# Kernel optimization log

Measured on AMD Instinct MI355X. Metric: run time of the kernel, lower is better.

## Reference

```python
import jax, jax.numpy as jnp
import numpy as np

B, T, D = 4, 2048, 1024
H, K, V = 4, 256, 256        # head_k_dim = head_v_dim = hidden/num_heads
M, TOPK = 256, 4             # num_slots == head_k_dim
CHUNK = 64                   # scan checkpointing granularity
SCALE = K ** -0.5            # kernel default q scale


def setup_inputs() -> dict:
    key = jax.random.key(0)
    ks = jax.random.split(key, 10)
    s = lambda i, shape, sc: jax.random.normal(ks[i], shape, jnp.float32) * sc
    return {
        "hidden_states": s(0, (B, T, D), 1.0),
        "Wq": s(1, (D, H * K), D ** -0.5),
        "Wk": s(2, (D, H * K), D ** -0.5),
        "Wv": s(3, (D, H * V), D ** -0.5),
        "Wa": s(4, (D, H), D ** -0.5),
        "Wr": s(5, (D, H * M), D ** -0.5),
        "Wb": s(6, (D, H), D ** -0.5),
        "dt": jax.random.uniform(ks[7], (H,), jnp.float32, np.log(0.001), np.log(0.1)),
        "norm_w": jnp.ones((V,), jnp.float32),
        "Wo": s(8, (H * V, D), (H * V) ** -0.5),
    }


def _l2norm(x):
    return x * jax.lax.rsqrt(jnp.sum(x * x, axis=-1, keepdims=True) + 1e-6)


def _delta_scan(q, k, v, g, beta):
    """Gated delta-rule recurrence. Time-major inputs:
    q,k,g: [T,B,H,K]; v: [T,B,H,V]; beta: [T,B,H]. Returns o: [T,B,H,V]."""
    def step(S, inp):
        qt, kt, vt, gt, bt = inp
        S = S * jnp.exp(gt)[..., None]                              # diag decay on key dim
        err = vt - jnp.einsum('bhk,bhkv->bhv', kt, S)               # delta-rule error
        S = S + kt[..., None] * (bt[..., None] * err)[..., None, :]
        o = jnp.einsum('bhk,bhkv->bhv', qt, S)
        return S, o

    @jax.checkpoint
    def chunk_fn(S, inp):
        return jax.lax.scan(step, S, inp)

    nc = T // CHUNK
    inp = tuple(x.reshape((nc, CHUNK) + x.shape[1:]) for x in (q, k, v, g, beta))
    S0 = jnp.zeros((B, H, K, V), jnp.float32)
    _, o = jax.lax.scan(chunk_fn, S0, inp)                          # o: [nc,CHUNK,B,H,V]
    return o.reshape((T,) + o.shape[2:])


def reference(hidden_states, Wq, Wk, Wv, Wa, Wr, Wb, dt, norm_w, Wo):
    h = hidden_states
    q = jax.nn.silu(h @ Wq).reshape(B, T, H, K)
    k = jax.nn.silu(h @ Wk).reshape(B, T, H, K)
    v = jax.nn.silu(h @ Wv).reshape(B, T, H, V)
    a = -jax.nn.softplus(h @ Wa) * jnp.exp(dt)                      # [B,T,H] log-decay magnitude
    rt = (h @ Wr).reshape(B, T, H, M)
    beta = jax.nn.sigmoid(h @ Wb)                                   # [B,T,H]

    # noisy top-k slot routing (eval: no noise)
    m = jax.nn.sigmoid(rt)
    w, idx = jax.lax.top_k(m, TOPK)                                 # [B,T,H,TOPK]
    mask = jnp.sum(jax.nn.one_hot(idx, M, dtype=m.dtype) * w[..., None], axis=-2)
    r = mask / (jnp.sum(mask, axis=-1, keepdims=True) + 1e-6)
    g = a[..., None] * r                                            # [B,T,H,K] (M == K)

    k = k * (1.0 - jnp.exp(g))
    q = _l2norm(q) * SCALE
    k = _l2norm(k)

    tm = lambda x: jnp.moveaxis(x, 1, 0)
    o = _delta_scan(tm(q), tm(k), tm(v), tm(g), tm(beta))           # [T,B,H,V]
    o = jnp.moveaxis(o, 0, 1)                                       # [B,T,H,V]

    # RMSNorm on head_v_dim (fp32, eps 1e-5)
    o = o * jax.lax.rsqrt(jnp.mean(o * o, axis=-1, keepdims=True) + 1e-5) * norm_w
    return o.reshape(B, T, H * V) @ Wo
```

## Files before the change

### kernel.cpp

```cpp
#include <hip/hip_runtime.h>
#include <hip/hip_bf16.h>

#define TT 2048
#define BB 4
#define HH 4
#define DD 1024

using bf16x8 = __attribute__((ext_vector_type(8))) short;
using f32x4  = __attribute__((ext_vector_type(4))) float;

__device__ __forceinline__ float wave_sum(float x) {
#pragma unroll
  for (int off = 32; off >= 1; off >>= 1) x += __shfl_xor(x, off);
  return x;
}

__device__ __forceinline__ float siluf(float x) {
  return x / (1.f + expf(-x));
}

__device__ __forceinline__ unsigned short f2bf(float f) {
  unsigned u = __float_as_uint(f);
  u = (u + 0x7fffu + ((u >> 16) & 1u)) >> 16;
  return (unsigned short)u;
}
__device__ __forceinline__ float bf2f(unsigned short b) {
  return __uint_as_float(((unsigned)b) << 16);
}
__device__ __forceinline__ unsigned pack2(float a, float b) {
  return ((unsigned)f2bf(a)) | (((unsigned)f2bf(b)) << 16);
}

__device__ __forceinline__ void gload_lds16(const void* g, void* l) {
  __builtin_amdgcn_global_load_lds(
      (const __attribute__((address_space(1))) unsigned int*)g,
      (__attribute__((address_space(3))) unsigned int*)l, 16, 0, 0);
}

#define LBAR()                                              \
  do {                                                      \
    asm volatile("s_waitcnt lgkmcnt(0)" ::: "memory");      \
    __builtin_amdgcn_s_barrier();                           \
    __builtin_amdgcn_sched_barrier(0);                      \
  } while (0)

__global__ __launch_bounds__(256) void gemm_bt(const unsigned short* __restrict__ A,
                                               const unsigned short* __restrict__ Bt,
                                               float* __restrict__ C,
                                               int M, int N, int K) {
  __shared__ unsigned short As[128 * 64];
  __shared__ unsigned short Bs[128 * 64];
  const int tid = threadIdx.x;
  const int l = tid & 63;
  const int w = tid >> 6;
  const int wm = w >> 1, wn = w & 1;
  const int bid = blockIdx.x;
  const int nt = N >> 7;
  const int swz = (bid & 7) * ((int)gridDim.x >> 3) + (bid >> 3);
  const int m0 = (swz / nt) * 128, n0 = (swz % nt) * 128;

  f32x4 acc[4][4];
#pragma unroll
  for (int i = 0; i < 4; ++i)
#pragma unroll
    for (int j = 0; j < 4; ++j) acc[i][j] = (f32x4){0.f, 0.f, 0.f, 0.f};

  size_t asrc[4], bsrc[4];
  int ldst[4];
#pragma unroll
  for (int it = 0; it < 4; ++it) {
    int chunk = (it * 4 + w) * 64 + l;
    int row = chunk >> 3, s = chunk & 7;
    size_t soff = (size_t)row * K + ((s ^ (row & 7)) << 3);
    asrc[it] = (size_t)m0 * K + soff;
    bsrc[it] = (size_t)n0 * K + soff;
    ldst[it] = chunk * 8;
  }
  int ra_off[2][4], rb_off[2][4];
#pragma unroll
  for (int kh = 0; kh < 2; ++kh)
#pragma unroll
    for (int f = 0; f < 4; ++f) {
      int rowA = wm * 64 + f * 16 + (l & 15);
      ra_off[kh][f] = rowA * 128 + (((kh * 4 + (l >> 4)) ^ (rowA & 7)) << 4);
      int rowB = wn * 64 + f * 16 + (l & 15);
      rb_off[kh][f] = rowB * 128 + (((kh * 4 + (l >> 4)) ^ (rowB & 7)) << 4);
    }

  for (int k0 = 0; k0 < K; k0 += 64) {
    __syncthreads();
#pragma unroll
    for (int it = 0; it < 4; ++it) {
      gload_lds16(A + asrc[it] + k0, As + ldst[it] - l * 8);
      gload_lds16(Bt + bsrc[it] + k0, Bs + ldst[it] - l * 8);
    }
    __syncthreads();
#pragma unroll
    for (int kh = 0; kh < 2; ++kh) {
      bf16x8 af[4], bfv[4];
#pragma unroll
      for (int f = 0; f < 4; ++f) {
        af[f] = *(const bf16x8*)((const char*)As + ra_off[kh][f]);
        bfv[f] = *(const bf16x8*)((const char*)Bs + rb_off[kh][f]);
      }
#pragma unroll
      for (int i = 0; i < 4; ++i)
#pragma unroll
        for (int j = 0; j < 4; ++j)
          acc[i][j] = __builtin_amdgcn_mfma_f32_16x16x32_bf16(af[i], bfv[j],
                                                              acc[i][j], 0, 0, 0);
    }
  }
  const int cn = n0 + wn * 64 + (l & 15);
  const int rbase = m0 + wm * 64 + ((l >> 4) << 2);
#pragma unroll
  for (int i = 0; i < 4; ++i)
#pragma unroll
    for (int j = 0; j < 4; ++j)
#pragma unroll
      for (int r = 0; r < 4; ++r)
        C[(size_t)(rbase + i * 16 + r) * N + cn + j * 16] = acc[i][j][r];
}

__global__ __launch_bounds__(256) void gemm_bt3(const unsigned short* __restrict__ Ah,
                                                const unsigned short* __restrict__ Al,
                                                const unsigned short* __restrict__ Bh,
                                                const unsigned short* __restrict__ Bl,
                                                float* __restrict__ C,
                                                int M, int N, int K) {
  __shared__ unsigned short Ash[128 * 64];
  __shared__ unsigned short Asl[128 * 64];
  __shared__ unsigned short Bsh[128 * 64];
  __shared__ unsigned short Bsl[128 * 64];
  const int tid = threadIdx.x;
  const int l = tid & 63;
  const int w = tid >> 6;
  const int wm = w >> 1, wn = w & 1;
  const int bid = blockIdx.x;
  const int nt = N >> 7;
  const int swz = (bid & 7) * ((int)gridDim.x >> 3) + (bid >> 3);
  const int m0 = (swz / nt) * 128, n0 = (swz % nt) * 128;

  f32x4 acc[4][4];
#pragma unroll
  for (int i = 0; i < 4; ++i)
#pragma unroll
    for (int j = 0; j < 4; ++j) acc[i][j] = (f32x4){0.f, 0.f, 0.f, 0.f};

  size_t asrc[4], bsrc[4];
  int ldst[4];
#pragma unroll
  for (int it = 0; it < 4; ++it) {
    int chunk = (it * 4 + w) * 64 + l;
    int row = chunk >> 3, s = chunk & 7;
    size_t soff = (size_t)row * K + ((s ^ (row & 7)) << 3);
    asrc[it] = (size_t)m0 * K + soff;
    bsrc[it] = (size_t)n0 * K + soff;
    ldst[it] = chunk * 8;
  }
  int ra_off[2][4], rb_off[2][4];
#pragma unroll
  for (int kh = 0; kh < 2; ++kh)
#pragma unroll
    for (int f = 0; f < 4; ++f) {
      int rowA = wm * 64 + f * 16 + (l & 15);
      ra_off[kh][f] = rowA * 128 + (((kh * 4 + (l >> 4)) ^ (rowA & 7)) << 4);
      int rowB = wn * 64 + f * 16 + (l & 15);
      rb_off[kh][f] = rowB * 128 + (((kh * 4 + (l >> 4)) ^ (rowB & 7)) << 4);
    }

  for (int k0 = 0; k0 < K; k0 += 64) {
    __syncthreads();
#pragma unroll
    for (int it = 0; it < 4; ++it) {
      gload_lds16(Ah + asrc[it] + k0, Ash + ldst[it] - l * 8);
      gload_lds16(Al + asrc[it] + k0, Asl + ldst[it] - l * 8);
      gload_lds16(Bh + bsrc[it] + k0, Bsh + ldst[it] - l * 8);
      gload_lds16(Bl + bsrc[it] + k0, Bsl + ldst[it] - l * 8);
    }
    __syncthreads();
#pragma unroll
    for (int kh = 0; kh < 2; ++kh) {
      bf16x8 afh[4], bfh[4], tmp[4];
#pragma unroll
      for (int f = 0; f < 4; ++f) {
        afh[f] = *(const bf16x8*)((const char*)Ash + ra_off[kh][f]);
        bfh[f] = *(const bf16x8*)((const char*)Bsh + rb_off[kh][f]);
      }
#pragma unroll
      for (int i = 0; i < 4; ++i)
#pragma unroll
        for (int j = 0; j < 4; ++j)
          acc[i][j] = __builtin_amdgcn_mfma_f32_16x16x32_bf16(afh[i], bfh[j],
                                                              acc[i][j], 0, 0, 0);
#pragma unroll
      for (int f = 0; f < 4; ++f)
        tmp[f] = *(const bf16x8*)((const char*)Asl + ra_off[kh][f]);
#pragma unroll
      for (int i = 0; i < 4; ++i)
#pragma unroll
        for (int j = 0; j < 4; ++j)
          acc[i][j] = __builtin_amdgcn_mfma_f32_16x16x32_bf16(tmp[i], bfh[j],
                                                              acc[i][j], 0, 0, 0);
#pragma unroll
      for (int f = 0; f < 4; ++f)
        tmp[f] = *(const bf16x8*)((const char*)Bsl + rb_off[kh][f]);
#pragma unroll
      for (int i = 0; i < 4; ++i)
#pragma unroll
        for (int j = 0; j < 4; ++j)
          acc[i][j] = __builtin_amdgcn_mfma_f32_16x16x32_bf16(afh[i], tmp[j],
                                                              acc[i][j], 0, 0, 0);
    }
  }
  const int cn = n0 + wn * 64 + (l & 15);
  const int rbase = m0 + wm * 64 + ((l >> 4) << 2);
#pragma unroll
  for (int i = 0; i < 4; ++i)
#pragma unroll
    for (int j = 0; j < 4; ++j)
#pragma unroll
      for (int r = 0; r < 4; ++r)
        C[(size_t)(rbase + i * 16 + r) * N + cn + j * 16] = acc[i][j][r];
}

__global__ __launch_bounds__(256) void cast_bf16_kernel(const float* __restrict__ in,
                                                        unsigned short* __restrict__ out) {
  const size_t i = ((size_t)blockIdx.x * 256 + threadIdx.x) * 4;
  float4 x = *(const float4*)(in + i);
  ushort4 o4;
  o4.x = f2bf(x.x);
  o4.y = f2bf(x.y);
  o4.z = f2bf(x.z);
  o4.w = f2bf(x.w);
  *(ushort4*)(out + i) = o4;
}

__global__ __launch_bounds__(256) void cast2_bf16_kernel(const float* __restrict__ in,
                                                         unsigned short* __restrict__ hi,
                                                         unsigned short* __restrict__ lo) {
  const size_t i = ((size_t)blockIdx.x * 256 + threadIdx.x) * 4;
  float4 x = *(const float4*)(in + i);
  ushort4 h4, l4;
  h4.x = f2bf(x.x); l4.x = f2bf(x.x - bf2f(h4.x));
  h4.y = f2bf(x.y); l4.y = f2bf(x.y - bf2f(h4.y));
  h4.z = f2bf(x.z); l4.z = f2bf(x.z - bf2f(h4.z));
  h4.w = f2bf(x.w); l4.w = f2bf(x.w - bf2f(h4.w));
  *(ushort4*)(hi + i) = h4;
  *(ushort4*)(lo + i) = l4;
}

__global__ __launch_bounds__(256) void tcast_kernel(const float* __restrict__ W,
                                                    unsigned short* __restrict__ WT,
                                                    int R, int C) {
  __shared__ float tile[32][33];
  const int tx = threadIdx.x, ty = threadIdx.y;
  const int c0 = blockIdx.x * 32, r0 = blockIdx.y * 32;
#pragma unroll
  for (int i = 0; i < 4; ++i)
    tile[ty + 8 * i][tx] = W[(size_t)(r0 + ty + 8 * i) * C + c0 + tx];
  __syncthreads();
#pragma unroll
  for (int i = 0; i < 4; ++i)
    WT[(size_t)(c0 + ty + 8 * i) * R + r0 + tx] = f2bf(tile[tx][ty + 8 * i]);
}

__global__ __launch_bounds__(256) void tcast2_kernel(const float* __restrict__ W,
                                                     unsigned short* __restrict__ WTh,
                                                     unsigned short* __restrict__ WTl,
                                                     int R, int C) {
  __shared__ float tile[32][33];
  const int tx = threadIdx.x, ty = threadIdx.y;
  const int c0 = blockIdx.x * 32, r0 = blockIdx.y * 32;
#pragma unroll
  for (int i = 0; i < 4; ++i)
    tile[ty + 8 * i][tx] = W[(size_t)(r0 + ty + 8 * i) * C + c0 + tx];
  __syncthreads();
#pragma unroll
  for (int i = 0; i < 4; ++i) {
    float x = tile[tx][ty + 8 * i];
    unsigned short h = f2bf(x);
    WTh[(size_t)(c0 + ty + 8 * i) * R + r0 + tx] = h;
    WTl[(size_t)(c0 + ty + 8 * i) * R + r0 + tx] = f2bf(x - bf2f(h));
  }
}

__global__ __launch_bounds__(256) void routing_kernel(
    const float* __restrict__ hidden, const float* __restrict__ Wa,
    const float* __restrict__ Wb, const float* __restrict__ dt,
    const float* __restrict__ rproj, float* __restrict__ qk,
    float* __restrict__ kk_, float* __restrict__ vv, float* __restrict__ gbuf,
    float* __restrict__ betaT) {
  const int row = blockIdx.x;
  const int b = row >> 11;
  const int t = row & (TT - 1);
  const int h = threadIdx.x >> 6;
  const int l = threadIdx.x & 63;
  const size_t base = (size_t)row * DD + h * 256;

  const float* hrow = hidden + (size_t)row * DD;
  float aa = 0.f, bb = 0.f;
#pragma unroll
  for (int i = 0; i < 16; ++i) {
    float hv = hrow[l + 64 * i];
    aa = fmaf(hv, Wa[(l + 64 * i) * HH + h], aa);
    bb = fmaf(hv, Wb[(l + 64 * i) * HH + h], bb);
  }
  aa = wave_sum(aa);
  bb = wave_sum(bb);
  float sp = (aa > 20.f) ? aa : log1pf(expf(aa));
  float a_ = -sp * expf(dt[h]);
  float beta = 1.f / (1.f + expf(-bb));
  const int bh = b * HH + h;
  if (l == 0) betaT[(size_t)bh * TT + t] = beta;

  float4 rt4 = *(const float4*)(rproj + base + l * 4);
  float rv[4] = {rt4.x, rt4.y, rt4.z, rt4.w};
  int used = 0;
  int widx[4];
  float wsig[4], wg[4], wkfac[4];
#pragma unroll
  for (int it = 0; it < 4; ++it) {
    float bv = -3.4e38f;
    int bi = 0x7fffffff;
#pragma unroll
    for (int c = 0; c < 4; ++c) {
      bool ok = !(used & (1 << c));
      float v = rv[c];
      if (ok && (v > bv)) {
        bv = v;
        bi = l * 4 + c;
      }
    }
#pragma unroll
    for (int off = 32; off >= 1; off >>= 1) {
      float ov = __shfl_xor(bv, off);
      int oi = __shfl_xor(bi, off);
      if (ov > bv || (ov == bv && oi < bi)) {
        bv = ov;
        bi = oi;
      }
    }
    widx[it] = bi;
    wsig[it] = 1.f / (1.f + expf(-bv));
    if ((bi >> 2) == l) used |= 1 << (bi & 3);
  }
  float wsum = wsig[0] + wsig[1] + wsig[2] + wsig[3] + 1e-6f;
#pragma unroll
  for (int it = 0; it < 4; ++it) {
    float g = a_ * (wsig[it] / wsum);
    wg[it] = g;
    wkfac[it] = 1.f - expf(g);
  }

  float4 kv4 = *(const float4*)(kk_ + base + l * 4);
  float kvv[4] = {kv4.x, kv4.y, kv4.z, kv4.w};
  float kmask[4], ddv[4];
#pragma unroll
  for (int c = 0; c < 4; ++c) {
    int slot = l * 4 + c;
    float f = 0.f, d = 0.f;
#pragma unroll
    for (int it = 0; it < 4; ++it) {
      bool hit = (slot == widx[it]);
      f = hit ? wkfac[it] : f;
      d = hit ? wg[it] : d;
    }
    kmask[c] = siluf(kvv[c]) * f;
    ddv[c] = d;
  }
  float ss = kmask[0] * kmask[0] + kmask[1] * kmask[1] + kmask[2] * kmask[2] +
             kmask[3] * kmask[3];
  ss = wave_sum(ss);
  float kn = rsqrtf(ss + 1e-6f);
  *(float4*)(kk_ + base + l * 4) =
      make_float4(kmask[0] * kn, kmask[1] * kn, kmask[2] * kn, kmask[3] * kn);
  *(float4*)(gbuf + ((size_t)bh * TT + t) * 256 + l * 4) =
      make_float4(ddv[0], ddv[1], ddv[2], ddv[3]);

  float4 qv4 = *(const float4*)(qk + base + l * 4);
  float qs[4] = {siluf(qv4.x), siluf(qv4.y), siluf(qv4.z), siluf(qv4.w)};
  float qss = qs[0] * qs[0] + qs[1] * qs[1] + qs[2] * qs[2] + qs[3] * qs[3];
  qss = wave_sum(qss);
  float qn = rsqrtf(qss + 1e-6f) * 0.0625f;
  *(float4*)(qk + base + l * 4) =
      make_float4(qs[0] * qn, qs[1] * qn, qs[2] * qn, qs[3] * qn);

  float4 vv4 = *(const float4*)(vv + base + l * 4);
  *(float4*)(vv + base + l * 4) =
      make_float4(siluf(vv4.x), siluf(vv4.y), siluf(vv4.z), siluf(vv4.w));
}

__global__ __launch_bounds__(256) void phaseA_kernel(
    const float* __restrict__ kproj, const float* __restrict__ qproj,
    float* __restrict__ expcG,
    const float* __restrict__ betaT, unsigned short* __restrict__ TinvB,
    unsigned short* __restrict__ AB, unsigned short* __restrict__ Wg,
    unsigned short* __restrict__ Qg, unsigned short* __restrict__ XTg) {
  __shared__ unsigned short XB[64 * 256];
  __shared__ unsigned short QW[128 * 256];
  __shared__ float Mb[64 * 68];
  const int bid = blockIdx.x;
  const int bh = bid >> 5, c = bid & 31;
  const int b = bh >> 2, h = bh & 3;
  const int t0 = c * 64;
  const int tid = threadIdx.x;
  const int w = tid >> 6, l = tid & 63;
  const int ln = l & 15, lg = l >> 4;

  {
    float cacc = 0.f;
    const int slot = tid >> 3, byt = tid & 7;
#pragma unroll 4
    for (int i = 0; i < 64; ++i) {
      size_t ga = ((size_t)bh * TT + t0 + i) * 256 + tid;
      size_t pa = (((size_t)b * TT + t0 + i) * HH + h) * 256 + tid;
      cacc += expcG[ga];
      float e = expf(cacc);
      float ei = __builtin_amdgcn_rcpf(e);
      float kv = kproj[pa], qv = qproj[pa];
      unsigned short wb = f2bf(kv * e);
      unsigned short qb = f2bf(qv * e);
      unsigned short xb = f2bf(kv * ei);
      Wg[ga] = wb;
      Qg[ga] = qb;
      int sw = ((slot ^ (i & 7)) << 3) + byt;
      XB[i * 256 + sw] = xb;
      QW[i * 256 + sw] = qb;
      QW[(i + 64) * 256 + sw] = wb;
      if (i == 63) expcG[ga] = e;
    }
  }
  __syncthreads();

  f32x4 acc[2][4];
#pragma unroll
  for (int tr = 0; tr < 2; ++tr)
#pragma unroll
    for (int tc = 0; tc < 4; ++tc) acc[tr][tc] = (f32x4){0.f, 0.f, 0.f, 0.f};
  const int R0 = w * 32;
#pragma unroll
  for (int kt = 0; kt < 8; ++kt) {
    const int ks = kt * 4 + lg;
    const int ra0 = R0 + ln, ra1 = R0 + 16 + ln;
    bf16x8 a0 = *(const bf16x8*)&QW[ra0 * 256 + ((ks ^ (ra0 & 7)) << 3)];
    bf16x8 a1 = *(const bf16x8*)&QW[ra1 * 256 + ((ks ^ (ra1 & 7)) << 3)];
#pragma unroll
    for (int tc = 0; tc < 4; ++tc) {
      const int br = tc * 16 + ln;
      bf16x8 bf_ = *(const bf16x8*)&XB[br * 256 + ((ks ^ (br & 7)) << 3)];
      acc[0][tc] = __builtin_amdgcn_mfma_f32_16x16x32_bf16(a0, bf_, acc[0][tc], 0, 0, 0);
      acc[1][tc] = __builtin_amdgcn_mfma_f32_16x16x32_bf16(a1, bf_, acc[1][tc], 0, 0, 0);
    }
  }
  const size_t gb = (((size_t)bh * 32 + c) << 12);
  if (w < 2) {
#pragma unroll
    for (int tr = 0; tr < 2; ++tr)
#pragma unroll
      for (int tc = 0; tc < 4; ++tc)
#pragma unroll
        for (int r = 0; r < 4; ++r) {
          int i = R0 + tr * 16 + lg * 4 + r;
          int s = tc * 16 + ln;
          AB[gb + i * 64 + s] = (s <= i) ? f2bf(acc[tr][tc][r]) : (unsigned short)0;
        }
  } else {
#pragma unroll
    for (int tr = 0; tr < 2; ++tr)
#pragma unroll
      for (int tc = 0; tc < 4; ++tc)
#pragma unroll
        for (int r = 0; r < 4; ++r) {
          int i = R0 - 64 + tr * 16 + lg * 4 + r;
          Mb[i * 68 + tc * 16 + ln] = acc[tr][tc][r];
        }
  }
  __syncthreads();

  if (w == 0) {
    float tcol[64];
#pragma unroll
    for (int i = 0; i < 64; ++i) {
      float bi = betaT[(size_t)bh * TT + t0 + i];
      float a_ = (l == i) ? 1.f : 0.f;
#pragma unroll
      for (int s = 0; s < i; ++s)
        a_ = fmaf(-bi * Mb[i * 68 + s], tcol[s], a_);
      tcol[i] = a_;
    }
#pragma unroll
    for (int s = 0; s < 64; ++s) Mb[s * 68 + l] = tcol[s];
  } else {
    const int kk1 = tid - 64;
#pragma unroll 1
    for (int pass = 0; pass < 2; ++pass) {
      if (pass == 1 && kk1 >= 64) break;
      const int k = (pass == 0) ? kk1 : (192 + kk1);
      unsigned short* dst = XTg + ((size_t)bh * 256 + k) * TT + t0;
      const int kslot = k >> 3, kb = k & 7;
#pragma unroll 1
      for (int jq = 0; jq < 8; ++jq) {
        unsigned short e[8];
#pragma unroll
        for (int j = 0; j < 8; ++j) {
          int t = jq * 8 + j;
          e[j] = XB[t * 256 + (((kslot ^ (t & 7)) << 3) + kb)];
        }
        uint4 o;
        o.x = ((unsigned)e[0]) | (((unsigned)e[1]) << 16);
        o.y = ((unsigned)e[2]) | (((unsigned)e[3]) << 16);
        o.z = ((unsigned)e[4]) | (((unsigned)e[5]) << 16);
        o.w = ((unsigned)e[6]) | (((unsigned)e[7]) << 16);
        *(uint4*)(dst + jq * 8) = o;
      }
    }
  }
  __syncthreads();
  {
    const int i = tid >> 2;
    const int sb = (tid & 3) * 16;
#pragma unroll
    for (int mq = 0; mq < 4; ++mq) {
      float v0 = Mb[i * 68 + sb + mq * 4 + 0];
      float v1 = Mb[i * 68 + sb + mq * 4 + 1];
      float v2 = Mb[i * 68 + sb + mq * 4 + 2];
      float v3 = Mb[i * 68 + sb + mq * 4 + 3];
      uint2 p;
      p.x = pack2(v0, v1);
      p.y = pack2(v2, v3);
      *(uint2*)(TinvB + gb + (size_t)i * 64 + sb + mq * 4) = p;
    }
  }
}

__global__ __launch_bounds__(256) void chunk_scan_kernel(
    const unsigned short* __restrict__ Wg, const unsigned short* __restrict__ Qg,
    const unsigned short* __restrict__ XTg, const unsigned short* __restrict__ Tb,
    const unsigned short* __restrict__ Ab, const float* __restrict__ vproj,
    const float* __restrict__ expcG, const float* __restrict__ betaT,
    float* __restrict__ obuf) {
  __shared__ unsigned short ShL[16 * 256];
  __shared__ unsigned short SlL[16 * 256];
  __shared__ unsigned short R2bL[16 * 64];
  __shared__ unsigned short UbL[16 * 64];
  const int bid = blockIdx.x;
  const int bh = bid & 15, slice = bid >> 4;
  const int b = bh >> 2, h = bh & 3;
  const int tid = threadIdx.x;
  const int w = tid >> 6;
  const int l = tid & 63;
  const int ln = l & 15, lg = l >> 4;

  const unsigned short* Wbh = Wg + (size_t)bh * TT * 256;
  const unsigned short* Qbh = Qg + (size_t)bh * TT * 256;
  const unsigned short* XTbh = XTg + (size_t)bh * 256 * TT;
  const unsigned short* Tbh = Tb + (size_t)bh * 32 * 4096;
  const unsigned short* Abh = Ab + (size_t)bh * 32 * 4096;
  const float* betabh = betaT + (size_t)bh * TT;
  const float* ebh = expcG + (size_t)bh * TT * 256;

  f32x4 S0 = {0.f, 0.f, 0.f, 0.f}, S1 = S0, S2 = S0, S3 = S0;

  const int ru_off =
      ln * 64 + ((((w * 2) + (lg >> 1)) ^ (ln & 7)) << 3) + (lg & 1) * 4;

  bf16x8 wA[8], qA[8], wB[8], qB[8];
  float4 vA, bA, vB, bB;

#define LOADWQV(W_, Q_, V_, B_, c_)                                            \
  {                                                                            \
    const int t0_ = (c_) * 64;                                                 \
    _Pragma("unroll") for (int kt = 0; kt < 8; ++kt) {                         \
      const size_t arow =                                                      \
          (size_t)(t0_ + w * 16 + ln) * 256 + kt * 32 + lg * 8;                \
      W_[kt] = *(const bf16x8*)(Wbh + arow);                                   \
      Q_[kt] = *(const bf16x8*)(Qbh + arow);                                   \
    }                                                                          \
    const size_t vrow =                                                        \
        ((size_t)(b * TT + t0_ + w * 16 + lg * 4) * HH + h) * 256 +            \
        slice * 16 + ln;                                                       \
    V_.x = vproj[vrow];                                                        \
    V_.y = vproj[vrow + HH * 256];                                             \
    V_.z = vproj[vrow + 2 * HH * 256];                                         \
    V_.w = vproj[vrow + 3 * HH * 256];                                         \
    B_ = *(const float4*)(betabh + t0_ + w * 16 + lg * 4);                     \
  }

#define SSTORE(S_, E_, mt_)                                                    \
  {                                                                            \
    S_[0] *= E_.x;                                                             \
    S_[1] *= E_.y;                                                             \
    S_[2] *= E_.z;                                                             \
    S_[3] *= E_.w;                                                             \
    ushort4 hp, lp;                                                            \
    hp.x = f2bf(S_[0]); lp.x = f2bf(S_[0] - bf2f(hp.x));                       \
    hp.y = f2bf(S_[1]); lp.y = f2bf(S_[1] - bf2f(hp.y));                       \
    hp.z = f2bf(S_[2]); lp.z = f2bf(S_[2] - bf2f(hp.z));                       \
    hp.w = f2bf(S_[3]); lp.w = f2bf(S_[3] - bf2f(hp.w));                       \
    const int so_ = ln * 256 +                                                 \
                    ((((w * 8) + (mt_)*2 + (lg >> 1)) ^ ln) << 3) +            \
                    (lg & 1) * 4;                                              \
    *(ushort4*)(&ShL[so_]) = hp;                                               \
    *(ushort4*)(&SlL[so_]) = lp;                                               \
  }

#define CHUNK(Wc, Qc, Vc, Bc, Wn, Qn, Vn, Bn, c_)                              \
  {                                                                            \
    const int c = (c_);                                                        \
    const size_t tb_base = (size_t)c * 4096 + (w * 16 + ln) * 64 + lg * 8;     \
    bf16x8 tf0 = *(const bf16x8*)(Tbh + tb_base);                              \
    bf16x8 tf1 = *(const bf16x8*)(Tbh + tb_base + 32);                         \
    bf16x8 af0 = *(const bf16x8*)(Abh + tb_base);                              \
    bf16x8 af1 = *(const bf16x8*)(Abh + tb_base + 32);                         \
    f32x4 rhs = {0.f, 0.f, 0.f, 0.f}, oq = {0.f, 0.f, 0.f, 0.f};               \
    if (c > 0) {                                                               \
      _Pragma("unroll") for (int kt = 0; kt < 8; ++kt) {                       \
        const int sro = ln * 256 + (((kt * 4 + lg) ^ ln) << 3);                \
        bf16x8 sh = *(const bf16x8*)(&ShL[sro]);                               \
        bf16x8 sl = *(const bf16x8*)(&SlL[sro]);                               \
        rhs = __builtin_amdgcn_mfma_f32_16x16x32_bf16(Wc[kt], sh, rhs, 0, 0, 0); \
        rhs = __builtin_amdgcn_mfma_f32_16x16x32_bf16(Wc[kt], sl, rhs, 0, 0, 0); \
        oq = __builtin_amdgcn_mfma_f32_16x16x32_bf16(Qc[kt], sh, oq, 0, 0, 0); \
        oq = __builtin_amdgcn_mfma_f32_16x16x32_bf16(Qc[kt], sl, oq, 0, 0, 0); \
      }                                                                        \
    }                                                                          \
    if (c + 1 < 32) LOADWQV(Wn, Qn, Vn, Bn, c + 1);                            \
    {                                                                          \
      ushort4 r2p;                                                             \
      r2p.x = f2bf(Bc.x * (Vc.x - rhs[0]));                                    \
      r2p.y = f2bf(Bc.y * (Vc.y - rhs[1]));                                    \
      r2p.z = f2bf(Bc.z * (Vc.z - rhs[2]));                                    \
      r2p.w = f2bf(Bc.w * (Vc.w - rhs[3]));                                    \
      *(ushort4*)(&R2bL[ru_off]) = r2p;                                        \
    }                                                                          \
    LBAR();                                                                    \
    bf16x8 xf0a, xf0b, xf1a, xf1b, xf2a, xf2b, xf3a, xf3b;                     \
    {                                                                          \
      const size_t xb = (size_t)(w * 64 + ln) * TT + c * 64 + lg * 8;          \
      xf0a = *(const bf16x8*)(XTbh + xb);                                      \
      xf0b = *(const bf16x8*)(XTbh + xb + 32);                                 \
      xf1a = *(const bf16x8*)(XTbh + xb + 16 * TT);                            \
      xf1b = *(const bf16x8*)(XTbh + xb + 16 * TT + 32);                       \
      xf2a = *(const bf16x8*)(XTbh + xb + 32 * TT);                            \
      xf2b = *(const bf16x8*)(XTbh + xb + 32 * TT + 32);                       \
      xf3a = *(const bf16x8*)(XTbh + xb + 48 * TT);                            \
      xf3b = *(const bf16x8*)(XTbh + xb + 48 * TT + 32);                       \
    }                                                                          \
    const float* ebase = ebh + (size_t)(c * 64 + 63) * 256 + w * 64 + lg * 4;  \
    float4 eL0 = *(const float4*)(ebase);                                      \
    float4 eL1 = *(const float4*)(ebase + 16);                                 \
    float4 eL2 = *(const float4*)(ebase + 32);                                 \
    float4 eL3 = *(const float4*)(ebase + 48);                                 \
    {                                                                          \
      bf16x8 rf0 = *(const bf16x8*)(&R2bL[ln * 64 + (((0 + lg) ^ (ln & 7)) << 3)]); \
      bf16x8 rf1 = *(const bf16x8*)(&R2bL[ln * 64 + (((4 + lg) ^ (ln & 7)) << 3)]); \
      f32x4 u = {0.f, 0.f, 0.f, 0.f};                                          \
      u = __builtin_amdgcn_mfma_f32_16x16x32_bf16(tf0, rf0, u, 0, 0, 0);       \
      u = __builtin_amdgcn_mfma_f32_16x16x32_bf16(tf1, rf1, u, 0, 0, 0);       \
      ushort4 up;                                                              \
      up.x = f2bf(u[0]);                                                       \
      up.y = f2bf(u[1]);                                                       \
      up.z = f2bf(u[2]);                                                       \
      up.w = f2bf(u[3]);                                                       \
      *(ushort4*)(&UbL[ru_off]) = up;                                          \
    }                                                                          \
    LBAR();                                                                    \
    bf16x8 uf0 = *(const bf16x8*)(&UbL[ln * 64 + (((0 + lg) ^ (ln & 7)) << 3)]); \
    bf16x8 uf1 = *(const bf16x8*)(&UbL[ln * 64 + (((4 + lg) ^ (ln & 7)) << 3)]); \
    {                                                                          \
      f32x4 o = oq;                                                            \
      o = __builtin_amdgcn_mfma_f32_16x16x32_bf16(af0, uf0, o, 0, 0, 0);       \
      o = __builtin_amdgcn_mfma_f32_16x16x32_bf16(af1, uf1, o, 0, 0, 0);       \
      const size_t orow =                                                      \
          ((size_t)(b * TT + c * 64 + w * 16 + lg * 4) * HH + h) * 256 +       \
          slice * 16 + ln;                                                     \
      obuf[orow] = o[0];                                                       \
      obuf[orow + HH * 256] = o[1];                                            \
      obuf[orow + 2 * HH * 256] = o[2];                                        \
      obuf[orow + 3 * HH * 256] = o[3];                                        \
    }                                                                          \
    S0 = __builtin_amdgcn_mfma_f32_16x16x32_bf16(xf0a, uf0, S0, 0, 0, 0);      \
    S0 = __builtin_amdgcn_mfma_f32_16x16x32_bf16(xf0b, uf1, S0, 0, 0, 0);      \
    S1 = __builtin_amdgcn_mfma_f32_16x16x32_bf16(xf1a, uf0, S1, 0, 0, 0);      \
    S1 = __builtin_amdgcn_mfma_f32_16x16x32_bf16(xf1b, uf1, S1, 0, 0, 0);      \
    S2 = __builtin_amdgcn_mfma_f32_16x16x32_bf16(xf2a, uf0, S2, 0, 0, 0);      \
    S2 = __builtin_amdgcn_mfma_f32_16x16x32_bf16(xf2b, uf1, S2, 0, 0, 0);      \
    S3 = __builtin_amdgcn_mfma_f32_16x16x32_bf16(xf3a, uf0, S3, 0, 0, 0);      \
    S3 = __builtin_amdgcn_mfma_f32_16x16x32_bf16(xf3b, uf1, S3, 0, 0, 0);      \
    SSTORE(S0, eL0, 0);                                                        \
    SSTORE(S1, eL1, 1);                                                        \
    SSTORE(S2, eL2, 2);                                                        \
    SSTORE(S3, eL3, 3);                                                        \
    LBAR();                                                                    \
  }

  LOADWQV(wA, qA, vA, bA, 0);
  for (int cc = 0; cc < 32; cc += 2) {
    CHUNK(wA, qA, vA, bA, wB, qB, vB, bB, cc);
    CHUNK(wB, qB, vB, bB, wA, qA, vA, bA, cc + 1);
  }
#undef CHUNK
#undef SSTORE
#undef LOADWQV
}

__global__ __launch_bounds__(256) void rmsnorm_kernel(
    const float* __restrict__ o, const float* __restrict__ w,
    float* __restrict__ out) {
  const int row = blockIdx.x;
  const int l = threadIdx.x & 63;
  const size_t base = (size_t)row * DD + (threadIdx.x >> 6) * 256 + l * 4;
  float4 x = *(const float4*)(o + base);
  float ss = x.x * x.x + x.y * x.y + x.z * x.z + x.w * x.w;
  ss = wave_sum(ss);
  float sc = rsqrtf(ss * (1.f / 256.f) + 1e-5f);
  float4 wv = *(const float4*)(w + l * 4);
  *(float4*)(out + base) = make_float4(x.x * sc * wv.x, x.y * sc * wv.y,
                                       x.z * sc * wv.z, x.w * sc * wv.w);
}

extern "C" void kernel_launch(void* const* d_in, const int* in_sizes, int n_in,
                              void* d_out, int out_size, void* d_ws,
                              size_t ws_size, hipStream_t stream) {
  const float* hidden = (const float*)d_in[0];
  const float* Wq = (const float*)d_in[1];
  const float* Wk = (const float*)d_in[2];
  const float* Wv = (const float*)d_in[3];
  const float* Wa = (const float*)d_in[4];
  const float* Wr = (const float*)d_in[5];
  const float* Wb = (const float*)d_in[6];
  const float* dt = (const float*)d_in[7];
  const float* norm_w = (const float*)d_in[8];
  const float* Wo = (const float*)d_in[9];
  float* out = (float*)d_out;

  const size_t NP = (size_t)BB * TT * DD;
  float* ws = (float*)d_ws;
  float* qproj = ws;
  float* kproj = ws + NP;
  float* vproj = ws + 2 * NP;
  float* gbuf = ws + 3 * NP;
  unsigned short* hbf = (unsigned short*)(ws + 4 * NP);
  unsigned short* wT = (unsigned short*)(ws + 4 * NP + NP / 2);
  unsigned short* WT0 = wT;
  unsigned short* WT1 = wT + 1048576;
  unsigned short* WT2 = wT + 2 * 1048576;
  unsigned short* WT3 = wT + 3 * 1048576;
  unsigned short* WT4 = wT + 4 * 1048576;
  unsigned short* WT5 = wT + 5 * 1048576;
  float* betaT = ws + 4 * NP + NP / 2 + 3 * 1024 * 1024;
  float* after_beta = betaT + 16 * TT;
  unsigned short* Qg = (unsigned short*)after_beta;
  unsigned short* XTg = Qg + NP;
  unsigned short* Ab = XTg + NP;
  unsigned short* Wgb = hbf;
  unsigned short* Tbb = WT4;
  unsigned short* hlo = (unsigned short*)qproj;
  float* rproj = out;
  float* normed = qproj;

  dim3 bt(256);
  cast2_bf16_kernel<<<8192, 256, 0, stream>>>(hidden, hbf, hlo);
  dim3 tg(32, 32), tb(32, 8);
  tcast2_kernel<<<tg, tb, 0, stream>>>(Wr, WT4, WT5, 1024, 1024);
  tcast_kernel<<<tg, tb, 0, stream>>>(Wq, WT0, 1024, 1024);
  tcast_kernel<<<tg, tb, 0, stream>>>(Wk, WT1, 1024, 1024);
  tcast_kernel<<<tg, tb, 0, stream>>>(Wv, WT2, 1024, 1024);
  tcast_kernel<<<tg, tb, 0, stream>>>(Wo, WT3, 1024, 1024);

  const int GEMM_BLKS = 512;
  gemm_bt3<<<GEMM_BLKS, bt, 0, stream>>>(hbf, hlo, WT4, WT5, rproj, 8192, 1024, 1024);
  gemm_bt<<<GEMM_BLKS, bt, 0, stream>>>(hbf, WT0, qproj, 8192, 1024, 1024);
  gemm_bt<<<GEMM_BLKS, bt, 0, stream>>>(hbf, WT1, kproj, 8192, 1024, 1024);
  gemm_bt<<<GEMM_BLKS, bt, 0, stream>>>(hbf, WT2, vproj, 8192, 1024, 1024);

  routing_kernel<<<8192, 256, 0, stream>>>(hidden, Wa, Wb, dt, rproj, qproj,
                                           kproj, vproj, gbuf, betaT);
  phaseA_kernel<<<512, 256, 0, stream>>>(kproj, qproj, gbuf, betaT, Tbb, Ab,
                                         Wgb, Qg, XTg);
  chunk_scan_kernel<<<256, 256, 0, stream>>>(Wgb, Qg, XTg, Tbb, Ab, vproj,
                                             gbuf, betaT, out);
  rmsnorm_kernel<<<8192, 256, 0, stream>>>(out, norm_w, normed);
  cast_bf16_kernel<<<8192, 256, 0, stream>>>(normed, hbf);
  gemm_bt<<<GEMM_BLKS, bt, 0, stream>>>(hbf, WT3, out, 8192, 1024, 1024);
}
```

Baseline: 472.4 us.

## Split chunk scan into 8-column V slices and fuse RMSNorm with bf16 cast

The chunk scan grid doubles from 256 to 512 blocks. Each block now writes only 8 of the 16 V columns its MFMA tile computes, so half the lanes do wasted work but twice as many CUs take part. Double-buffered register prefetch is replaced by a single buffer, and launch_bounds(256,2) caps register use so two blocks can share a CU. RMSNorm now writes bf16 directly, which removes a separate cast kernel and an fp32 intermediate round trip.

```diff
diff --git a/kernel.cpp b/kernel.cpp
--- a/kernel.cpp
+++ b/kernel.cpp
@@ -222,18 +222,6 @@
 #pragma unroll
       for (int r = 0; r < 4; ++r)
         C[(size_t)(rbase + i * 16 + r) * N + cn + j * 16] = acc[i][j][r];
-}
-
-__global__ __launch_bounds__(256) void cast_bf16_kernel(const float* __restrict__ in,
-                                                        unsigned short* __restrict__ out) {
-  const size_t i = ((size_t)blockIdx.x * 256 + threadIdx.x) * 4;
-  float4 x = *(const float4*)(in + i);
-  ushort4 o4;
-  o4.x = f2bf(x.x);
-  o4.y = f2bf(x.y);
-  o4.z = f2bf(x.z);
-  o4.w = f2bf(x.w);
-  *(ushort4*)(out + i) = o4;
 }
 
 __global__ __launch_bounds__(256) void cast2_bf16_kernel(const float* __restrict__ in,
@@ -534,7 +522,7 @@
   }
 }
 
-__global__ __launch_bounds__(256) void chunk_scan_kernel(
+__global__ __launch_bounds__(256, 2) void chunk_scan_kernel(
     const unsigned short* __restrict__ Wg, const unsigned short* __restrict__ Qg,
     const unsigned short* __restrict__ XTg, const unsigned short* __restrict__ Tb,
     const unsigned short* __restrict__ Ab, const float* __restrict__ vproj,
@@ -551,6 +539,8 @@
   const int w = tid >> 6;
   const int l = tid & 63;
   const int ln = l & 15, lg = l >> 4;
+  int vcol = slice * 8 + ln;
+  if (vcol > 255) vcol = 255;
 
   const unsigned short* Wbh = Wg + (size_t)bh * TT * 256;
   const unsigned short* Qbh = Qg + (size_t)bh * TT * 256;
@@ -565,26 +555,25 @@
   const int ru_off =
       ln * 64 + ((((w * 2) + (lg >> 1)) ^ (ln & 7)) << 3) + (lg & 1) * 4;
 
-  bf16x8 wA[8], qA[8], wB[8], qB[8];
-  float4 vA, bA, vB, bB;
-
-#define LOADWQV(W_, Q_, V_, B_, c_)                                            \
+  bf16x8 wR[8], qR[8];
+  float4 vR, bR;
+
+#define LOADWQV(c_)                                                            \
   {                                                                            \
     const int t0_ = (c_) * 64;                                                 \
     _Pragma("unroll") for (int kt = 0; kt < 8; ++kt) {                         \
       const size_t arow =                                                      \
           (size_t)(t0_ + w * 16 + ln) * 256 + kt * 32 + lg * 8;                \
-      W_[kt] = *(const bf16x8*)(Wbh + arow);                                   \
-      Q_[kt] = *(const bf16x8*)(Qbh + arow);                                   \
+      wR[kt] = *(const bf16x8*)(Wbh + arow);                                   \
+      qR[kt] = *(const bf16x8*)(Qbh + arow);                                   \
     }                                                                          \
     const size_t vrow =                                                        \
-        ((size_t)(b * TT + t0_ + w * 16 + lg * 4) * HH + h) * 256 +            \
-        slice * 16 + ln;                                                       \
-    V_.x = vproj[vrow];                                                        \
-    V_.y = vproj[vrow + HH * 256];                                             \
-    V_.z = vproj[vrow + 2 * HH * 256];                                         \
-    V_.w = vproj[vrow + 3 * HH * 256];                                         \
-    B_ = *(const float4*)(betabh + t0_ + w * 16 + lg * 4);                     \
+        ((size_t)(b * TT + t0_ + w * 16 + lg * 4) * HH + h) * 256 + vcol;      \
+    vR.x = vproj[vrow];                                                        \
+    vR.y = vproj[vrow + HH * 256];                                             \
+    vR.z = vproj[vrow + 2 * HH * 256];                                         \
+    vR.w = vproj[vrow + 3 * HH * 256];                                         \
+    bR = *(const float4*)(betabh + t0_ + w * 16 + lg * 4);                     \
   }
 
 #define SSTORE(S_, E_, mt_)                                                    \
@@ -605,109 +594,104 @@
     *(ushort4*)(&SlL[so_]) = lp;                                               \
   }
 
-#define CHUNK(Wc, Qc, Vc, Bc, Wn, Qn, Vn, Bn, c_)                              \
-  {                                                                            \
-    const int c = (c_);                                                        \
-    const size_t tb_base = (size_t)c * 4096 + (w * 16 + ln) * 64 + lg * 8;     \
-    bf16x8 tf0 = *(const bf16x8*)(Tbh + tb_base);                              \
-    bf16x8 tf1 = *(const bf16x8*)(Tbh + tb_base + 32);                         \
-    bf16x8 af0 = *(const bf16x8*)(Abh + tb_base);                              \
-    bf16x8 af1 = *(const bf16x8*)(Abh + tb_base + 32);                         \
-    f32x4 rhs = {0.f, 0.f, 0.f, 0.f}, oq = {0.f, 0.f, 0.f, 0.f};               \
-    if (c > 0) {                                                               \
-      _Pragma("unroll") for (int kt = 0; kt < 8; ++kt) {                       \
-        const int sro = ln * 256 + (((kt * 4 + lg) ^ ln) << 3);                \
-        bf16x8 sh = *(const bf16x8*)(&ShL[sro]);                               \
-        bf16x8 sl = *(const bf16x8*)(&SlL[sro]);                               \
-        rhs = __builtin_amdgcn_mfma_f32_16x16x32_bf16(Wc[kt], sh, rhs, 0, 0, 0); \
-        rhs = __builtin_amdgcn_mfma_f32_16x16x32_bf16(Wc[kt], sl, rhs, 0, 0, 0); \
-        oq = __builtin_amdgcn_mfma_f32_16x16x32_bf16(Qc[kt], sh, oq, 0, 0, 0); \
-        oq = __builtin_amdgcn_mfma_f32_16x16x32_bf16(Qc[kt], sl, oq, 0, 0, 0); \
-      }                                                                        \
-    }                                                                          \
-    if (c + 1 < 32) LOADWQV(Wn, Qn, Vn, Bn, c + 1);                            \
-    {                                                                          \
-      ushort4 r2p;                                                             \
-      r2p.x = f2bf(Bc.x * (Vc.x - rhs[0]));                                    \
-      r2p.y = f2bf(Bc.y * (Vc.y - rhs[1]));                                    \
-      r2p.z = f2bf(Bc.z * (Vc.z - rhs[2]));                                    \
-      r2p.w = f2bf(Bc.w * (Vc.w - rhs[3]));                                    \
-      *(ushort4*)(&R2bL[ru_off]) = r2p;                                        \
-    }                                                                          \
-    LBAR();                                                                    \
-    bf16x8 xf0a, xf0b, xf1a, xf1b, xf2a, xf2b, xf3a, xf3b;                     \
-    {                                                                          \
-      const size_t xb = (size_t)(w * 64 + ln) * TT + c * 64 + lg * 8;          \
-      xf0a = *(const bf16x8*)(XTbh + xb);                                      \
-      xf0b = *(const bf16x8*)(XTbh + xb + 32);                                 \
-      xf1a = *(const bf16x8*)(XTbh + xb + 16 * TT);                            \
-      xf1b = *(const bf16x8*)(XTbh + xb + 16 * TT + 32);                       \
-      xf2a = *(const bf16x8*)(XTbh + xb + 32 * TT);                            \
-      xf2b = *(const bf16x8*)(XTbh + xb + 32 * TT + 32);                       \
-      xf3a = *(const bf16x8*)(XTbh + xb + 48 * TT);                            \
-      xf3b = *(const bf16x8*)(XTbh + xb + 48 * TT + 32);                       \
-    }                                                                          \
-    const float* ebase = ebh + (size_t)(c * 64 + 63) * 256 + w * 64 + lg * 4;  \
-    float4 eL0 = *(const float4*)(ebase);                                      \
-    float4 eL1 = *(const float4*)(ebase + 16);                                 \
-    float4 eL2 = *(const float4*)(ebase + 32);                                 \
-    float4 eL3 = *(const float4*)(ebase + 48);                                 \
-    {                                                                          \
-      bf16x8 rf0 = *(const bf16x8*)(&R2bL[ln * 64 + (((0 + lg) ^ (ln & 7)) << 3)]); \
-      bf16x8 rf1 = *(const bf16x8*)(&R2bL[ln * 64 + (((4 + lg) ^ (ln & 7)) << 3)]); \
-      f32x4 u = {0.f, 0.f, 0.f, 0.f};                                          \
-      u = __builtin_amdgcn_mfma_f32_16x16x32_bf16(tf0, rf0, u, 0, 0, 0);       \
-      u = __builtin_amdgcn_mfma_f32_16x16x32_bf16(tf1, rf1, u, 0, 0, 0);       \
-      ushort4 up;                                                              \
-      up.x = f2bf(u[0]);                                                       \
-      up.y = f2bf(u[1]);                                                       \
-      up.z = f2bf(u[2]);                                                       \
-      up.w = f2bf(u[3]);                                                       \
-      *(ushort4*)(&UbL[ru_off]) = up;                                          \
-    }                                                                          \
-    LBAR();                                                                    \
-    bf16x8 uf0 = *(const bf16x8*)(&UbL[ln * 64 + (((0 + lg) ^ (ln & 7)) << 3)]); \
-    bf16x8 uf1 = *(const bf16x8*)(&UbL[ln * 64 + (((4 + lg) ^ (ln & 7)) << 3)]); \
-    {                                                                          \
-      f32x4 o = oq;                                                            \
-      o = __builtin_amdgcn_mfma_f32_16x16x32_bf16(af0, uf0, o, 0, 0, 0);       \
-      o = __builtin_amdgcn_mfma_f32_16x16x32_bf16(af1, uf1, o, 0, 0, 0);       \
-      const size_t orow =                                                      \
-          ((size_t)(b * TT + c * 64 + w * 16 + lg * 4) * HH + h) * 256 +       \
-          slice * 16 + ln;                                                     \
-      obuf[orow] = o[0];                                                       \
-      obuf[orow + HH * 256] = o[1];                                            \
-      obuf[orow + 2 * HH * 256] = o[2];                                        \
-      obuf[orow + 3 * HH * 256] = o[3];                                        \
-    }                                                                          \
-    S0 = __builtin_amdgcn_mfma_f32_16x16x32_bf16(xf0a, uf0, S0, 0, 0, 0);      \
-    S0 = __builtin_amdgcn_mfma_f32_16x16x32_bf16(xf0b, uf1, S0, 0, 0, 0);      \
-    S1 = __builtin_amdgcn_mfma_f32_16x16x32_bf16(xf1a, uf0, S1, 0, 0, 0);      \
-    S1 = __builtin_amdgcn_mfma_f32_16x16x32_bf16(xf1b, uf1, S1, 0, 0, 0);      \
-    S2 = __builtin_amdgcn_mfma_f32_16x16x32_bf16(xf2a, uf0, S2, 0, 0, 0);      \
-    S2 = __builtin_amdgcn_mfma_f32_16x16x32_bf16(xf2b, uf1, S2, 0, 0, 0);      \
-    S3 = __builtin_amdgcn_mfma_f32_16x16x32_bf16(xf3a, uf0, S3, 0, 0, 0);      \
-    S3 = __builtin_amdgcn_mfma_f32_16x16x32_bf16(xf3b, uf1, S3, 0, 0, 0);      \
-    SSTORE(S0, eL0, 0);                                                        \
-    SSTORE(S1, eL1, 1);                                                        \
-    SSTORE(S2, eL2, 2);                                                        \
-    SSTORE(S3, eL3, 3);                                                        \
-    LBAR();                                                                    \
-  }
-
-  LOADWQV(wA, qA, vA, bA, 0);
-  for (int cc = 0; cc < 32; cc += 2) {
-    CHUNK(wA, qA, vA, bA, wB, qB, vB, bB, cc);
-    CHUNK(wB, qB, vB, bB, wA, qA, vA, bA, cc + 1);
-  }
-#undef CHUNK
+  LOADWQV(0);
+  for (int c = 0; c < 32; ++c) {
+    const size_t tb_base = (size_t)c * 4096 + (w * 16 + ln) * 64 + lg * 8;
+    bf16x8 tf0 = *(const bf16x8*)(Tbh + tb_base);
+    bf16x8 tf1 = *(const bf16x8*)(Tbh + tb_base + 32);
+    bf16x8 af0 = *(const bf16x8*)(Abh + tb_base);
+    bf16x8 af1 = *(const bf16x8*)(Abh + tb_base + 32);
+    f32x4 rhs = {0.f, 0.f, 0.f, 0.f}, oq = {0.f, 0.f, 0.f, 0.f};
+    if (c > 0) {
+#pragma unroll
+      for (int kt = 0; kt < 8; ++kt) {
+        const int sro = ln * 256 + (((kt * 4 + lg) ^ ln) << 3);
+        bf16x8 sh = *(const bf16x8*)(&ShL[sro]);
+        bf16x8 sl = *(const bf16x8*)(&SlL[sro]);
+        rhs = __builtin_amdgcn_mfma_f32_16x16x32_bf16(wR[kt], sh, rhs, 0, 0, 0);
+        rhs = __builtin_amdgcn_mfma_f32_16x16x32_bf16(wR[kt], sl, rhs, 0, 0, 0);
+        oq = __builtin_amdgcn_mfma_f32_16x16x32_bf16(qR[kt], sh, oq, 0, 0, 0);
+        oq = __builtin_amdgcn_mfma_f32_16x16x32_bf16(qR[kt], sl, oq, 0, 0, 0);
+      }
+    }
+    {
+      ushort4 r2p;
+      r2p.x = f2bf(bR.x * (vR.x - rhs[0]));
+      r2p.y = f2bf(bR.y * (vR.y - rhs[1]));
+      r2p.z = f2bf(bR.z * (vR.z - rhs[2]));
+      r2p.w = f2bf(bR.w * (vR.w - rhs[3]));
+      *(ushort4*)(&R2bL[ru_off]) = r2p;
+    }
+    if (c + 1 < 32) LOADWQV(c + 1);
+    LBAR();
+    bf16x8 xf0a, xf0b, xf1a, xf1b, xf2a, xf2b, xf3a, xf3b;
+    {
+      const size_t xb = (size_t)(w * 64 + ln) * TT + c * 64 + lg * 8;
+      xf0a = *(const bf16x8*)(XTbh + xb);
+      xf0b = *(const bf16x8*)(XTbh + xb + 32);
+      xf1a = *(const bf16x8*)(XTbh + xb + 16 * TT);
+      xf1b = *(const bf16x8*)(XTbh + xb + 16 * TT + 32);
+      xf2a = *(const bf16x8*)(XTbh + xb + 32 * TT);
+      xf2b = *(const bf16x8*)(XTbh + xb + 32 * TT + 32);
+      xf3a = *(const bf16x8*)(XTbh + xb + 48 * TT);
+      xf3b = *(const bf16x8*)(XTbh + xb + 48 * TT + 32);
+    }
+    const float* ebase = ebh + (size_t)(c * 64 + 63) * 256 + w * 64 + lg * 4;
+    float4 eL0 = *(const float4*)(ebase);
+    float4 eL1 = *(const float4*)(ebase + 16);
+    float4 eL2 = *(const float4*)(ebase + 32);
+    float4 eL3 = *(const float4*)(ebase + 48);
+    {
+      bf16x8 rf0 = *(const bf16x8*)(&R2bL[ln * 64 + (((0 + lg) ^ (ln & 7)) << 3)]);
+      bf16x8 rf1 = *(const bf16x8*)(&R2bL[ln * 64 + (((4 + lg) ^ (ln & 7)) << 3)]);
+      f32x4 u = {0.f, 0.f, 0.f, 0.f};
+      u = __builtin_amdgcn_mfma_f32_16x16x32_bf16(tf0, rf0, u, 0, 0, 0);
+      u = __builtin_amdgcn_mfma_f32_16x16x32_bf16(tf1, rf1, u, 0, 0, 0);
+      ushort4 up;
+      up.x = f2bf(u[0]);
+      up.y = f2bf(u[1]);
+      up.z = f2bf(u[2]);
+      up.w = f2bf(u[3]);
+      *(ushort4*)(&UbL[ru_off]) = up;
+    }
+    LBAR();
+    bf16x8 uf0 = *(const bf16x8*)(&UbL[ln * 64 + (((0 + lg) ^ (ln & 7)) << 3)]);
+    bf16x8 uf1 = *(const bf16x8*)(&UbL[ln * 64 + (((4 + lg) ^ (ln & 7)) << 3)]);
+    {
+      f32x4 o = oq;
+      o = __builtin_amdgcn_mfma_f32_16x16x32_bf16(af0, uf0, o, 0, 0, 0);
+      o = __builtin_amdgcn_mfma_f32_16x16x32_bf16(af1, uf1, o, 0, 0, 0);
+      if (ln < 8) {
+        const size_t orow =
+            ((size_t)(b * TT + c * 64 + w * 16 + lg * 4) * HH + h) * 256 +
+            slice * 8 + ln;
+        obuf[orow] = o[0];
+        obuf[orow + HH * 256] = o[1];
+        obuf[orow + 2 * HH * 256] = o[2];
+        obuf[orow + 3 * HH * 256] = o[3];
+      }
+    }
+    S0 = __builtin_amdgcn_mfma_f32_16x16x32_bf16(xf0a, uf0, S0, 0, 0, 0);
+    S0 = __builtin_amdgcn_mfma_f32_16x16x32_bf16(xf0b, uf1, S0, 0, 0, 0);
+    S1 = __builtin_amdgcn_mfma_f32_16x16x32_bf16(xf1a, uf0, S1, 0, 0, 0);
+    S1 = __builtin_amdgcn_mfma_f32_16x16x32_bf16(xf1b, uf1, S1, 0, 0, 0);
+    S2 = __builtin_amdgcn_mfma_f32_16x16x32_bf16(xf2a, uf0, S2, 0, 0, 0);
+    S2 = __builtin_amdgcn_mfma_f32_16x16x32_bf16(xf2b, uf1, S2, 0, 0, 0);
+    S3 = __builtin_amdgcn_mfma_f32_16x16x32_bf16(xf3a, uf0, S3, 0, 0, 0);
+    S3 = __builtin_amdgcn_mfma_f32_16x16x32_bf16(xf3b, uf1, S3, 0, 0, 0);
+    SSTORE(S0, eL0, 0);
+    SSTORE(S1, eL1, 1);
+    SSTORE(S2, eL2, 2);
+    SSTORE(S3, eL3, 3);
+    LBAR();
+  }
 #undef SSTORE
 #undef LOADWQV
 }
 
-__global__ __launch_bounds__(256) void rmsnorm_kernel(
+__global__ __launch_bounds__(256) void rmsnorm_bf16_kernel(
     const float* __restrict__ o, const float* __restrict__ w,
-    float* __restrict__ out) {
+    unsigned short* __restrict__ out) {
   const int row = blockIdx.x;
   const int l = threadIdx.x & 63;
   const size_t base = (size_t)row * DD + (threadIdx.x >> 6) * 256 + l * 4;
@@ -716,8 +700,12 @@
   ss = wave_sum(ss);
   float sc = rsqrtf(ss * (1.f / 256.f) + 1e-5f);
   float4 wv = *(const float4*)(w + l * 4);
-  *(float4*)(out + base) = make_float4(x.x * sc * wv.x, x.y * sc * wv.y,
-                                       x.z * sc * wv.z, x.w * sc * wv.w);
+  ushort4 o4;
+  o4.x = f2bf(x.x * sc * wv.x);
+  o4.y = f2bf(x.y * sc * wv.y);
+  o4.z = f2bf(x.z * sc * wv.z);
+  o4.w = f2bf(x.w * sc * wv.w);
+  *(ushort4*)(out + base) = o4;
 }
 
 extern "C" void kernel_launch(void* const* d_in, const int* in_sizes, int n_in,
@@ -758,7 +746,6 @@
   unsigned short* Tbb = WT4;
   unsigned short* hlo = (unsigned short*)qproj;
   float* rproj = out;
-  float* normed = qproj;
 
   dim3 bt(256);
   cast2_bf16_kernel<<<8192, 256, 0, stream>>>(hidden, hbf, hlo);
@@ -779,9 +766,8 @@
                                            kproj, vproj, gbuf, betaT);
   phaseA_kernel<<<512, 256, 0, stream>>>(kproj, qproj, gbuf, betaT, Tbb, Ab,
                                          Wgb, Qg, XTg);
-  chunk_scan_kernel<<<256, 256, 0, stream>>>(Wgb, Qg, XTg, Tbb, Ab, vproj,
+  chunk_scan_kernel<<<512, 256, 0, stream>>>(Wgb, Qg, XTg, Tbb, Ab, vproj,
                                              gbuf, betaT, out);
-  rmsnorm_kernel<<<8192, 256, 0, stream>>>(out, norm_w, normed);
-  cast_bf16_kernel<<<8192, 256, 0, stream>>>(normed, hbf);
+  rmsnorm_bf16_kernel<<<8192, 256, 0, stream>>>(out, norm_w, hbf);
   gemm_bt<<<GEMM_BLKS, bt, 0, stream>>>(hbf, WT3, out, 8192, 1024, 1024);
 }
```

Result: slower. 544.5 us (+15.3%).
